# Performance work log

Measured on AMD Instinct MI355X. Metric: run time of the kernel, lower is better.

Reference implementation:

```python
import jax, jax.numpy as jnp
import numpy as np

B, S, R = 1, 512, 384
C_MSA, C_Z, C_HID, N_HEAD = 64, 128, 32, 8
INF = 1e8


def layer_norm(x, gamma, beta, eps=1e-5):
    mu = jnp.mean(x, axis=-1, keepdims=True)
    var = jnp.mean(jnp.square(x - mu), axis=-1, keepdims=True)
    return (x - mu) * jax.lax.rsqrt(var + eps) * gamma + beta


def setup_inputs() -> dict:
    key = jax.random.key(0)
    ks = jax.random.split(key, 8)
    hc = N_HEAD * C_HID
    return {
        "m": jax.random.normal(ks[0], (B, S, R, C_MSA), jnp.float32),
        "z": jax.random.normal(ks[1], (B, R, R, C_Z), jnp.float32),
        "msa_mask": jnp.ones((B, S, R), jnp.float32),
        "z_mask": jnp.ones((B, R, R), jnp.float32),
        "ln_m_g": jnp.ones((C_MSA,), jnp.float32),
        "ln_m_b": jnp.zeros((C_MSA,), jnp.float32),
        "w_v": jax.random.normal(ks[2], (C_MSA, hc), jnp.float32) / np.sqrt(C_MSA),
        "w_g": jax.random.normal(ks[3], (C_MSA, hc), jnp.float32) * 0.02,
        "ln_z_g": jnp.ones((C_Z,), jnp.float32),
        "ln_z_b": jnp.zeros((C_Z,), jnp.float32),
        "w_b": jax.random.normal(ks[4], (C_Z, N_HEAD), jnp.float32) / np.sqrt(C_Z),
        "w_o": jax.random.normal(ks[5], (hc, C_MSA), jnp.float32) * 0.02,
    }


def reference(m, z, msa_mask, z_mask, ln_m_g, ln_m_b, w_v, w_g, ln_z_g, ln_z_b, w_b, w_o):
    b_, s_, r_ = m.shape[0], m.shape[1], m.shape[2]
    m_ln = layer_norm(m, ln_m_g, ln_m_b)                       # [B,S,R,Cm]
    v = (m_ln @ w_v).reshape(b_, s_, r_, N_HEAD, C_HID)        # [B,S,R,H,C]
    g = jax.nn.sigmoid(m_ln @ w_g).reshape(b_, s_, r_, N_HEAD, C_HID)
    bias = layer_norm(z, ln_z_g, ln_z_b) @ w_b                 # [B,R,R,H]
    bias = bias + INF * (z_mask[..., None] - 1.0)
    v = v * msa_mask[..., None, None]
    w = jax.nn.softmax(bias, axis=2)                           # softmax over j
    # weighted average over residues j, then sigmoid gating
    o = g * jnp.einsum('bijh,bsjhc->bsihc', w, v)              # [B,S,R,H,C]
    o = o.reshape(b_, s_, r_, N_HEAD * C_HID)
    return o @ w_o                                             # [B,S,R,Cm]
```

## Files before the change

### kernel.cpp

```cpp
#include <hip/hip_runtime.h>
#include <math.h>

#define S_DIM 512
#define R_DIM 384
#define CM 64
#define CZ 128
#define NH 8
#define CH 32
#define HC 256

typedef unsigned short u16;
typedef __attribute__((ext_vector_type(8))) __bf16 bf16x8;
typedef __attribute__((ext_vector_type(4))) float f32x4;

static __device__ __forceinline__ u16 f2bf(float f) {
    unsigned int u = __float_as_uint(f);
    unsigned int r = (u + 0x7fffu + ((u >> 16) & 1u)) >> 16;
    return (u16)r;
}
static __device__ __forceinline__ float bf2f(u16 h) {
    return __uint_as_float(((unsigned int)h) << 16);
}
static __device__ __forceinline__ void split2(float f, u16& hi, u16& lo) {
    hi = f2bf(f);
    lo = f2bf(f - bf2f(hi));
}

__global__ __launch_bounds__(256) void kW_prep(
    const float* __restrict__ wv, const float* __restrict__ wg,
    const float* __restrict__ wb,
    u16* __restrict__ wvT_hi, u16* __restrict__ wvT_lo,
    u16* __restrict__ wgT_hi, u16* __restrict__ wgT_lo,
    u16* __restrict__ wbT_hi, u16* __restrict__ wbT_lo)
{
    const int idx = blockIdx.x * 256 + threadIdx.x;
    if (idx < 16384) {
        const int n = idx >> 6, c = idx & 63;
        split2(wv[c * HC + n], wvT_hi[idx], wvT_lo[idx]);
    } else if (idx < 32768) {
        const int r = idx - 16384;
        const int n = r >> 6, c = r & 63;
        split2(wg[c * HC + n], wgT_hi[r], wgT_lo[r]);
    } else if (idx < 34816) {
        const int r = idx - 32768;
        const int n = r >> 7, c = r & 127;
        split2(n < NH ? wb[c * NH + n] : 0.f, wbT_hi[r], wbT_lo[r]);
    }
}

__global__ __launch_bounds__(256) void kA1_bias(
    const float* __restrict__ z, const float* __restrict__ z_mask,
    const float* __restrict__ ln_z_g, const float* __restrict__ ln_z_b,
    const u16* __restrict__ wbT_hi, const u16* __restrict__ wbT_lo,
    float* __restrict__ bias_ws)
{
    __shared__ __align__(16) u16 a_hi[128 * 136];
    __shared__ __align__(16) u16 a_lo[128 * 136];
    __shared__ __align__(16) u16 b_hi[16 * 136];
    __shared__ __align__(16) u16 b_lo[16 * 136];
    const int tid  = threadIdx.x;
    const int lane = tid & 63, w = tid >> 6;
    const int row0 = blockIdx.x * 128;

    {
        const int r = tid >> 1, half = tid & 1;
        const float* src = z + (size_t)(row0 + r) * CZ + half * 64;
        float x[64];
        float s1 = 0.f, s2 = 0.f;
        #pragma unroll
        for (int e = 0; e < 16; ++e) {
            float4 v4 = *reinterpret_cast<const float4*>(src + e * 4);
            x[e*4+0] = v4.x; x[e*4+1] = v4.y; x[e*4+2] = v4.z; x[e*4+3] = v4.w;
            s1 += v4.x + v4.y + v4.z + v4.w;
            s2 += v4.x*v4.x + v4.y*v4.y + v4.z*v4.z + v4.w*v4.w;
        }
        s1 += __shfl_xor(s1, 1);
        s2 += __shfl_xor(s2, 1);
        const float mu   = s1 * (1.f / CZ);
        const float var  = s2 * (1.f / CZ) - mu * mu;
        const float rstd = rsqrtf(var + 1e-5f);
        #pragma unroll
        for (int e = 0; e < 16; ++e) {
            float4 g4 = *reinterpret_cast<const float4*>(ln_z_g + half * 64 + e * 4);
            float4 b4 = *reinterpret_cast<const float4*>(ln_z_b + half * 64 + e * 4);
            const int c = half * 64 + e * 4;
            split2((x[e*4+0] - mu) * rstd * g4.x + b4.x,
                   a_hi[r * 136 + c + 0], a_lo[r * 136 + c + 0]);
            split2((x[e*4+1] - mu) * rstd * g4.y + b4.y,
                   a_hi[r * 136 + c + 1], a_lo[r * 136 + c + 1]);
            split2((x[e*4+2] - mu) * rstd * g4.z + b4.z,
                   a_hi[r * 136 + c + 2], a_lo[r * 136 + c + 2]);
            split2((x[e*4+3] - mu) * rstd * g4.w + b4.w,
                   a_hi[r * 136 + c + 3], a_lo[r * 136 + c + 3]);
        }
    }
    {
        const int row = tid >> 4, off = (tid & 15) * 8;
        *reinterpret_cast<uint4*>(&b_hi[row * 136 + off]) =
            *reinterpret_cast<const uint4*>(wbT_hi + row * 128 + off);
        *reinterpret_cast<uint4*>(&b_lo[row * 136 + off]) =
            *reinterpret_cast<const uint4*>(wbT_lo + row * 128 + off);
    }
    __syncthreads();

    const int wr = w * 32;
    f32x4 acc[2] = {};
    #pragma unroll
    for (int ks = 0; ks < 4; ++ks) {
        const int ko = ks * 32 + (lane >> 4) * 8;
        bf16x8 bh = *reinterpret_cast<const bf16x8*>(&b_hi[(lane & 15) * 136 + ko]);
        bf16x8 bl = *reinterpret_cast<const bf16x8*>(&b_lo[(lane & 15) * 136 + ko]);
        #pragma unroll
        for (int mm = 0; mm < 2; ++mm) {
            const int base = (wr + mm * 16 + (lane & 15)) * 136 + ko;
            bf16x8 ah = *reinterpret_cast<const bf16x8*>(&a_hi[base]);
            bf16x8 al = *reinterpret_cast<const bf16x8*>(&a_lo[base]);
            acc[mm] = __builtin_amdgcn_mfma_f32_16x16x32_bf16(ah, bh, acc[mm], 0, 0, 0);
            acc[mm] = __builtin_amdgcn_mfma_f32_16x16x32_bf16(al, bh, acc[mm], 0, 0, 0);
            acc[mm] = __builtin_amdgcn_mfma_f32_16x16x32_bf16(ah, bl, acc[mm], 0, 0, 0);
        }
    }

    __syncthreads();
    float* T = reinterpret_cast<float*>(a_hi);
    const int cl = lane & 15, r4 = (lane >> 4) * 4;
    #pragma unroll
    for (int mm = 0; mm < 2; ++mm) {
        if (cl < NH) {
            #pragma unroll
            for (int r = 0; r < 4; ++r)
                T[cl * 132 + wr + mm * 16 + r4 + r] = acc[mm][r];
        }
    }
    __syncthreads();
    {
        const int h = tid >> 5, q = (tid & 31) * 4;
        float4 v  = *reinterpret_cast<const float4*>(&T[h * 132 + q]);
        float4 mk = *reinterpret_cast<const float4*>(z_mask + row0 + q);
        v.x += 1e8f * (mk.x - 1.f);
        v.y += 1e8f * (mk.y - 1.f);
        v.z += 1e8f * (mk.z - 1.f);
        v.w += 1e8f * (mk.w - 1.f);
        *reinterpret_cast<float4*>(
            &bias_ws[(size_t)h * R_DIM * R_DIM + row0 + q]) = v;
    }
}

__global__ __launch_bounds__(256) void kA2_softmax(
    const float* __restrict__ bias_ws, u16* __restrict__ w_soft)
{
    const int tid = threadIdx.x, w = tid >> 6, lane = tid & 63;
    const int row = blockIdx.x * 4 + w;
    const float* src = bias_ws + (size_t)row * R_DIM;
    float vals[6];
    float mx = -1e30f;
    #pragma unroll
    for (int u = 0; u < 6; ++u) {
        vals[u] = src[lane + u * 64];
        mx = fmaxf(mx, vals[u]);
    }
    #pragma unroll
    for (int msk = 32; msk >= 1; msk >>= 1) mx = fmaxf(mx, __shfl_xor(mx, msk));
    float sum = 0.f;
    #pragma unroll
    for (int u = 0; u < 6; ++u) { vals[u] = __expf(vals[u] - mx); sum += vals[u]; }
    #pragma unroll
    for (int msk = 32; msk >= 1; msk >>= 1) sum += __shfl_xor(sum, msk);
    const float inv = 1.0f / sum;
    u16* dst = w_soft + (size_t)row * R_DIM;
    #pragma unroll
    for (int u = 0; u < 6; ++u)
        dst[lane + u * 64] = f2bf(vals[u] * inv);
}

__global__ __launch_bounds__(256) void kB_mfma(
    const float* __restrict__ m_chunk, const float* __restrict__ mask_chunk,
    const float* __restrict__ ln_g, const float* __restrict__ ln_b,
    const u16* __restrict__ wvT_hi, const u16* __restrict__ wvT_lo,
    const u16* __restrict__ wgT_hi, const u16* __restrict__ wgT_lo,
    u16* __restrict__ Vt, u16* __restrict__ gbuf, int SCH)
{
    __shared__ __align__(16) u16 smem[4 * 128 * 72];
    u16* a_hi = smem;
    u16* a_lo = smem + 128 * 72;
    u16* b_hi = smem + 2 * 128 * 72;
    u16* b_lo = smem + 3 * 128 * 72;
    const int tid   = threadIdx.x;
    const int panel = blockIdx.x;
    const int si0   = blockIdx.y * 128;
    const int n0    = (panel & 1) * 128;
    const int lane  = tid & 63;
    const int w     = tid >> 6;
    const int wr    = (w >> 1) * 64, wc = (w & 1) * 64;

    {
        const int r = tid >> 1, half = tid & 1;
        const float* src = m_chunk + (size_t)(si0 + r) * CM + half * 32;
        float x[32];
        float s1 = 0.f, s2 = 0.f;
        #pragma unroll
        for (int e = 0; e < 8; ++e) {
            float4 v4 = *reinterpret_cast<const float4*>(src + e * 4);
            x[e*4+0] = v4.x; x[e*4+1] = v4.y; x[e*4+2] = v4.z; x[e*4+3] = v4.w;
            s1 += v4.x + v4.y + v4.z + v4.w;
            s2 += v4.x*v4.x + v4.y*v4.y + v4.z*v4.z + v4.w*v4.w;
        }
        s1 += __shfl_xor(s1, 1);
        s2 += __shfl_xor(s2, 1);
        const float mu   = s1 * (1.f / 64);
        const float var  = s2 * (1.f / 64) - mu * mu;
        const float rstd = rsqrtf(var + 1e-5f);
        #pragma unroll
        for (int e = 0; e < 8; ++e) {
            #pragma unroll
            for (int q = 0; q < 4; ++q) {
                const int c = half * 32 + e * 4 + q;
                const float v = (x[e*4+q] - mu) * rstd * ln_g[c] + ln_b[c];
                split2(v, a_hi[r * 72 + c], a_lo[r * 72 + c]);
            }
        }
    }
    {
        const u16* Wh = (panel < 2 ? wvT_hi : wgT_hi) + (size_t)n0 * 64;
        const u16* Wl = (panel < 2 ? wvT_lo : wgT_lo) + (size_t)n0 * 64;
        #pragma unroll
        for (int e = 0; e < 4; ++e) {
            const int c = e * 256 + tid;
            const int row = c >> 3, off = (c & 7) * 8;
            *reinterpret_cast<uint4*>(&b_hi[row * 72 + off]) =
                *reinterpret_cast<const uint4*>(Wh + row * 64 + off);
            *reinterpret_cast<uint4*>(&b_lo[row * 72 + off]) =
                *reinterpret_cast<const uint4*>(Wl + row * 64 + off);
        }
    }
    __syncthreads();

    f32x4 acc[4][4] = {};
    #pragma unroll
    for (int ks = 0; ks < 2; ++ks) {
        const int ko = ks * 32 + (lane >> 4) * 8;
        bf16x8 ah[4], al[4], bh[4], bl[4];
        #pragma unroll
        for (int mm = 0; mm < 4; ++mm) {
            const int base = (wr + mm * 16 + (lane & 15)) * 72 + ko;
            ah[mm] = *reinterpret_cast<const bf16x8*>(&a_hi[base]);
            al[mm] = *reinterpret_cast<const bf16x8*>(&a_lo[base]);
        }
        #pragma unroll
        for (int nn = 0; nn < 4; ++nn) {
            const int base = (wc + nn * 16 + (lane & 15)) * 72 + ko;
            bh[nn] = *reinterpret_cast<const bf16x8*>(&b_hi[base]);
            bl[nn] = *reinterpret_cast<const bf16x8*>(&b_lo[base]);
        }
        #pragma unroll
        for (int mm = 0; mm < 4; ++mm)
            #pragma unroll
            for (int nn = 0; nn < 4; ++nn) {
                acc[mm][nn] = __builtin_amdgcn_mfma_f32_16x16x32_bf16(
                    ah[mm], bh[nn], acc[mm][nn], 0, 0, 0);
                acc[mm][nn] = __builtin_amdgcn_mfma_f32_16x16x32_bf16(
                    al[mm], bh[nn], acc[mm][nn], 0, 0, 0);
                acc[mm][nn] = __builtin_amdgcn_mfma_f32_16x16x32_bf16(
                    ah[mm], bl[nn], acc[mm][nn], 0, 0, 0);
            }
    }

    __syncthreads();
    const int r4 = (lane >> 4) * 4, cl = lane & 15;
    if (panel < 2) {
        u16* T = smem;
        #pragma unroll
        for (int mm = 0; mm < 4; ++mm) {
            const int rowb = wr + mm * 16 + r4;
            const float4 mk = *reinterpret_cast<const float4*>(mask_chunk + si0 + rowb);
            #pragma unroll
            for (int nn = 0; nn < 4; ++nn) {
                const int n = wc + nn * 16 + cl;
                ushort4 pk;
                pk.x = f2bf(acc[mm][nn][0] * mk.x);
                pk.y = f2bf(acc[mm][nn][1] * mk.y);
                pk.z = f2bf(acc[mm][nn][2] * mk.z);
                pk.w = f2bf(acc[mm][nn][3] * mk.w);
                *reinterpret_cast<ushort4*>(&T[n * 136 + rowb]) = pk;
            }
        }
        __syncthreads();
        const int sc = si0 / R_DIM, j0 = si0 % R_DIM;
        const size_t Nn = (size_t)SCH * 32;
        #pragma unroll
        for (int e = 0; e < 8; ++e) {
            const int c = e * 256 + tid;
            const int n = c >> 4, part = c & 15;
            const int k = n0 + n;
            const int h = k >> 5, cc = k & 31;
            u16* dst = Vt + ((size_t)h * Nn + (size_t)sc * 32 + cc) * R_DIM
                         + j0 + part * 8;
            *reinterpret_cast<uint4*>(dst) =
                *reinterpret_cast<const uint4*>(&T[n * 136 + part * 8]);
        }
    } else {
        u16* T = smem;
        #pragma unroll
        for (int mm = 0; mm < 4; ++mm) {
            const int rowb = wr + mm * 16 + r4;
            #pragma unroll
            for (int nn = 0; nn < 4; ++nn) {
                const int n = wc + nn * 16 + cl;
                #pragma unroll
                for (int r = 0; r < 4; ++r)
                    T[(rowb + r) * 136 + n] =
                        f2bf(1.f / (1.f + __expf(-acc[mm][nn][r])));
            }
        }
        __syncthreads();
        #pragma unroll
        for (int e = 0; e < 8; ++e) {
            const int c = e * 256 + tid;
            const int row = c >> 4, part = c & 15;
            u16* dst = gbuf + (size_t)(si0 + row) * HC + n0 + part * 8;
            *reinterpret_cast<uint4*>(dst) =
                *reinterpret_cast<const uint4*>(&T[row * 136 + part * 8]);
        }
    }
}

__global__ __launch_bounds__(256) void kC_mfma(
    const u16* __restrict__ Wsoft, const u16* __restrict__ Vt,
    u16* __restrict__ o_pre, int SCH)
{
    constexpr int LDSP = 40;
    __shared__ __align__(16) u16 lds_a[128 * LDSP];
    __shared__ __align__(16) u16 lds_b[128 * LDSP];
    const int N   = SCH * 32;
    const int n0  = blockIdx.x * 128;
    const int i0  = blockIdx.y * 128;
    const int h   = blockIdx.z;
    const int tid = threadIdx.x;
    const int lane = tid & 63;
    const int w    = tid >> 6;
    const int wr   = (w >> 1) * 64;
    const int wc   = (w & 1) * 64;

    const u16* Wp = Wsoft + (size_t)h * R_DIM * R_DIM;
    const u16* Vp = Vt    + (size_t)h * N * R_DIM;

    f32x4 acc[4][4] = {};

    for (int k0 = 0; k0 < R_DIM; k0 += 32) {
        __syncthreads();
        #pragma unroll
        for (int rep = 0; rep < 2; ++rep) {
            const int c = rep * 256 + tid;
            const int row = c >> 2, q = c & 3;
            uint4 va = *reinterpret_cast<const uint4*>(
                Wp + (size_t)(i0 + row) * R_DIM + k0 + q * 8);
            *reinterpret_cast<uint4*>(&lds_a[row * LDSP + q * 8]) = va;
            uint4 vb = *reinterpret_cast<const uint4*>(
                Vp + (size_t)(n0 + row) * R_DIM + k0 + q * 8);
            *reinterpret_cast<uint4*>(&lds_b[row * LDSP + q * 8]) = vb;
        }
        __syncthreads();

        bf16x8 afrag[4], bfrag[4];
        #pragma unroll
        for (int mm = 0; mm < 4; ++mm) {
            const int row = wr + mm * 16 + (lane & 15);
            afrag[mm] = *reinterpret_cast<const bf16x8*>(
                &lds_a[row * LDSP + (lane >> 4) * 8]);
        }
        #pragma unroll
        for (int nn = 0; nn < 4; ++nn) {
            const int row = wc + nn * 16 + (lane & 15);
            bfrag[nn] = *reinterpret_cast<const bf16x8*>(
                &lds_b[row * LDSP + (lane >> 4) * 8]);
        }
        #pragma unroll
        for (int mm = 0; mm < 4; ++mm)
            #pragma unroll
            for (int nn = 0; nn < 4; ++nn)
                acc[mm][nn] = __builtin_amdgcn_mfma_f32_16x16x32_bf16(
                    afrag[mm], bfrag[nn], acc[mm][nn], 0, 0, 0);
    }

    const int r4 = (lane >> 4) * 4;
    const int cl = lane & 15;
    #pragma unroll
    for (int mm = 0; mm < 4; ++mm) {
        #pragma unroll
        for (int nn = 0; nn < 4; ++nn) {
            const int i = i0 + wr + mm * 16 + r4;
            const int n = n0 + wc + nn * 16 + cl;
            const int sc = n >> 5, cc = n & 31;
            u16* dst = &o_pre[((size_t)sc * R_DIM + i) * HC + h * 32 + cc];
            #pragma unroll
            for (int r = 0; r < 4; ++r)
                dst[(size_t)r * HC] = f2bf(acc[mm][nn][r]);
        }
    }
}

__global__ __launch_bounds__(256) void kD_out(
    const u16* __restrict__ gbuf, const u16* __restrict__ o_pre,
    const float* __restrict__ w_o, float* __restrict__ out_chunk, int SCH)
{
    __shared__ float A[128 * 65];
    __shared__ float Bt[64 * 64];
    const int si0 = blockIdx.x * 128;
    const int tid = threadIdx.x;
    const int tx  = tid & 15, ty = tid >> 4;
    float acc[8][4] = {};

    for (int k0 = 0; k0 < HC; k0 += 64) {
        {
            const int r = tid >> 1, half = tid & 1;
            const size_t base = (size_t)(si0 + r) * HC + k0 + half * 32;
            float* dst = &A[r * 65 + half * 32];
            #pragma unroll
            for (int e = 0; e < 4; ++e) {
                uint4 gv = *reinterpret_cast<const uint4*>(gbuf + base + e * 8);
                uint4 ov = *reinterpret_cast<const uint4*>(o_pre + base + e * 8);
                const u16* ga = (const u16*)&gv;
                const u16* oa = (const u16*)&ov;
                #pragma unroll
                for (int q = 0; q < 8; ++q)
                    dst[e * 8 + q] = bf2f(ga[q]) * bf2f(oa[q]);
            }
        }
        {
            const int kk = tid >> 2, q = tid & 3;
            #pragma unroll
            for (int e = 0; e < 4; ++e) {
                float4 v4 = *reinterpret_cast<const float4*>(
                    w_o + (size_t)(k0 + kk) * CM + q * 16 + e * 4);
                *reinterpret_cast<float4*>(&Bt[kk * 64 + q * 16 + e * 4]) = v4;
            }
        }
        __syncthreads();
        #pragma unroll 8
        for (int kk = 0; kk < 64; ++kk) {
            float4 b = *reinterpret_cast<float4*>(&Bt[kk * 64 + tx * 4]);
            #pragma unroll
            for (int e = 0; e < 8; ++e) {
                float a = A[(ty * 8 + e) * 65 + kk];
                acc[e][0] += a * b.x; acc[e][1] += a * b.y;
                acc[e][2] += a * b.z; acc[e][3] += a * b.w;
            }
        }
        __syncthreads();
    }
    #pragma unroll
    for (int e = 0; e < 8; ++e) {
        *reinterpret_cast<float4*>(
            &out_chunk[(size_t)(si0 + ty * 8 + e) * CM + tx * 4]) =
            make_float4(acc[e][0], acc[e][1], acc[e][2], acc[e][3]);
    }
}

extern "C" void kernel_launch(void* const* d_in, const int* in_sizes, int n_in,
                              void* d_out, int out_size, void* d_ws, size_t ws_size,
                              hipStream_t stream)
{
    const float* m        = (const float*)d_in[0];
    const float* z        = (const float*)d_in[1];
    const float* msa_mask = (const float*)d_in[2];
    const float* z_mask   = (const float*)d_in[3];
    const float* ln_m_g   = (const float*)d_in[4];
    const float* ln_m_b   = (const float*)d_in[5];
    const float* w_v      = (const float*)d_in[6];
    const float* w_g      = (const float*)d_in[7];
    const float* ln_z_g   = (const float*)d_in[8];
    const float* ln_z_b   = (const float*)d_in[9];
    const float* w_b      = (const float*)d_in[10];
    const float* w_o      = (const float*)d_in[11];
    float* out = (float*)d_out;

    const size_t wsoft_bytes = (size_t)NH * R_DIM * R_DIM * 2;
    const size_t bias_bytes  = (size_t)NH * R_DIM * R_DIM * 4;
    const size_t wts_bytes   = 4 * 16384 * 2 + 2 * 2048 * 2;
    const size_t per_sch = (size_t)R_DIM * HC * (2 + 2 + 2);
    int SCH = 256;
    while (SCH > 4 &&
           wsoft_bytes + bias_bytes + wts_bytes + (size_t)SCH * per_sch > ws_size)
        SCH >>= 1;

    char* p = (char*)d_ws;
    u16* w_soft   = (u16*)p; p += wsoft_bytes;
    float* biasws = (float*)p; p += bias_bytes;
    u16* wvT_hi   = (u16*)p; p += 16384 * 2;
    u16* wvT_lo   = (u16*)p; p += 16384 * 2;
    u16* wgT_hi   = (u16*)p; p += 16384 * 2;
    u16* wgT_lo   = (u16*)p; p += 16384 * 2;
    u16* wbT_hi   = (u16*)p; p += 2048 * 2;
    u16* wbT_lo   = (u16*)p; p += 2048 * 2;
    u16* Vt       = (u16*)p; p += (size_t)SCH * 32 * NH * R_DIM * 2;
    u16* gbuf     = (u16*)p; p += (size_t)SCH * R_DIM * HC * 2;
    u16* obuf     = (u16*)p;

    kW_prep<<<136, 256, 0, stream>>>(w_v, w_g, w_b, wvT_hi, wvT_lo,
                                     wgT_hi, wgT_lo, wbT_hi, wbT_lo);
    kA1_bias<<<R_DIM * R_DIM / 128, 256, 0, stream>>>(
        z, z_mask, ln_z_g, ln_z_b, wbT_hi, wbT_lo, biasws);
    kA2_softmax<<<NH * R_DIM / 4, 256, 0, stream>>>(biasws, w_soft);

    for (int s0 = 0; s0 < S_DIM; s0 += SCH) {
        kB_mfma<<<dim3(4, SCH * 3), 256, 0, stream>>>(
            m + (size_t)s0 * R_DIM * CM, msa_mask + (size_t)s0 * R_DIM,
            ln_m_g, ln_m_b, wvT_hi, wvT_lo, wgT_hi, wgT_lo, Vt, gbuf, SCH);
        kC_mfma<<<dim3(SCH / 4, 3, NH), 256, 0, stream>>>(w_soft, Vt, obuf, SCH);
        kD_out<<<dim3(SCH * 3), 256, 0, stream>>>(gbuf, obuf, w_o,
                                                  out + (size_t)s0 * R_DIM * CM, SCH);
    }
}
```

Before: 328.1 us.

## Compute LayerNorm once per row tile and loop all four V/G panels in-block

Each kB block now normalizes its 128 rows of m once, then loops over the four V and gate output panels. Before, four separate blocks each re-read and re-normalized the same rows. Weight fragments are read straight from global memory instead of being staged in LDS, and the normalized activations are packed in registers and written to LDS as vector stores. This cuts redundant m traffic and LayerNorm work by four times, but the grid shrinks by four, which may leave compute units idle and serializes the panels inside each block.

```diff
diff --git a/kernel.cpp b/kernel.cpp
--- a/kernel.cpp
+++ b/kernel.cpp
@@ -180,18 +180,14 @@
     const u16* __restrict__ wgT_hi, const u16* __restrict__ wgT_lo,
     u16* __restrict__ Vt, u16* __restrict__ gbuf, int SCH)
 {
-    __shared__ __align__(16) u16 smem[4 * 128 * 72];
-    u16* a_hi = smem;
-    u16* a_lo = smem + 128 * 72;
-    u16* b_hi = smem + 2 * 128 * 72;
-    u16* b_lo = smem + 3 * 128 * 72;
-    const int tid   = threadIdx.x;
-    const int panel = blockIdx.x;
-    const int si0   = blockIdx.y * 128;
-    const int n0    = (panel & 1) * 128;
-    const int lane  = tid & 63;
-    const int w     = tid >> 6;
-    const int wr    = (w >> 1) * 64, wc = (w & 1) * 64;
+    __shared__ __align__(16) u16 a_hi[128 * 72];
+    __shared__ __align__(16) u16 a_lo[128 * 72];
+    __shared__ __align__(16) u16 Tbuf[128 * 136];
+    const int tid  = threadIdx.x;
+    const int si0  = blockIdx.x * 128;
+    const int lane = tid & 63;
+    const int w    = tid >> 6;
+    const int wr   = (w >> 1) * 64, wc = (w & 1) * 64;
 
     {
         const int r = tid >> 1, half = tid & 1;
@@ -210,116 +206,121 @@
         const float mu   = s1 * (1.f / 64);
         const float var  = s2 * (1.f / 64) - mu * mu;
         const float rstd = rsqrtf(var + 1e-5f);
+        u16 ph[32], pl[32];
         #pragma unroll
         for (int e = 0; e < 8; ++e) {
             #pragma unroll
             for (int q = 0; q < 4; ++q) {
-                const int c = half * 32 + e * 4 + q;
-                const float v = (x[e*4+q] - mu) * rstd * ln_g[c] + ln_b[c];
-                split2(v, a_hi[r * 72 + c], a_lo[r * 72 + c]);
-            }
-        }
-    }
-    {
-        const u16* Wh = (panel < 2 ? wvT_hi : wgT_hi) + (size_t)n0 * 64;
-        const u16* Wl = (panel < 2 ? wvT_lo : wgT_lo) + (size_t)n0 * 64;
+                const int cl_ = e * 4 + q;
+                const int c = half * 32 + cl_;
+                const float v = (x[cl_] - mu) * rstd * ln_g[c] + ln_b[c];
+                split2(v, ph[cl_], pl[cl_]);
+            }
+        }
+        u16* dh = &a_hi[r * 72 + half * 32];
+        u16* dl = &a_lo[r * 72 + half * 32];
         #pragma unroll
         for (int e = 0; e < 4; ++e) {
-            const int c = e * 256 + tid;
-            const int row = c >> 3, off = (c & 7) * 8;
-            *reinterpret_cast<uint4*>(&b_hi[row * 72 + off]) =
-                *reinterpret_cast<const uint4*>(Wh + row * 64 + off);
-            *reinterpret_cast<uint4*>(&b_lo[row * 72 + off]) =
-                *reinterpret_cast<const uint4*>(Wl + row * 64 + off);
+            *reinterpret_cast<uint4*>(dh + e * 8) =
+                reinterpret_cast<const uint4*>(ph)[e];
+            *reinterpret_cast<uint4*>(dl + e * 8) =
+                reinterpret_cast<const uint4*>(pl)[e];
         }
     }
     __syncthreads();
 
-    f32x4 acc[4][4] = {};
-    #pragma unroll
-    for (int ks = 0; ks < 2; ++ks) {
-        const int ko = ks * 32 + (lane >> 4) * 8;
-        bf16x8 ah[4], al[4], bh[4], bl[4];
-        #pragma unroll
-        for (int mm = 0; mm < 4; ++mm) {
-            const int base = (wr + mm * 16 + (lane & 15)) * 72 + ko;
-            ah[mm] = *reinterpret_cast<const bf16x8*>(&a_hi[base]);
-            al[mm] = *reinterpret_cast<const bf16x8*>(&a_lo[base]);
-        }
-        #pragma unroll
-        for (int nn = 0; nn < 4; ++nn) {
-            const int base = (wc + nn * 16 + (lane & 15)) * 72 + ko;
-            bh[nn] = *reinterpret_cast<const bf16x8*>(&b_hi[base]);
-            bl[nn] = *reinterpret_cast<const bf16x8*>(&b_lo[base]);
-        }
-        #pragma unroll
-        for (int mm = 0; mm < 4; ++mm)
+    #pragma unroll
+    for (int t = 0; t < 4; ++t) {
+        const int n0   = (t & 1) * 128;
+        const bool isV = (t < 2);
+        const u16* Wh = (isV ? wvT_hi : wgT_hi) + (size_t)n0 * 64;
+        const u16* Wl = (isV ? wvT_lo : wgT_lo) + (size_t)n0 * 64;
+
+        f32x4 acc[4][4] = {};
+        #pragma unroll
+        for (int ks = 0; ks < 2; ++ks) {
+            const int ko = ks * 32 + (lane >> 4) * 8;
+            bf16x8 ah[4], al[4], bh[4], bl[4];
             #pragma unroll
             for (int nn = 0; nn < 4; ++nn) {
-                acc[mm][nn] = __builtin_amdgcn_mfma_f32_16x16x32_bf16(
-                    ah[mm], bh[nn], acc[mm][nn], 0, 0, 0);
-                acc[mm][nn] = __builtin_amdgcn_mfma_f32_16x16x32_bf16(
-                    al[mm], bh[nn], acc[mm][nn], 0, 0, 0);
-                acc[mm][nn] = __builtin_amdgcn_mfma_f32_16x16x32_bf16(
-                    ah[mm], bl[nn], acc[mm][nn], 0, 0, 0);
-            }
-    }
-
-    __syncthreads();
-    const int r4 = (lane >> 4) * 4, cl = lane & 15;
-    if (panel < 2) {
-        u16* T = smem;
-        #pragma unroll
-        for (int mm = 0; mm < 4; ++mm) {
-            const int rowb = wr + mm * 16 + r4;
-            const float4 mk = *reinterpret_cast<const float4*>(mask_chunk + si0 + rowb);
-            #pragma unroll
-            for (int nn = 0; nn < 4; ++nn) {
-                const int n = wc + nn * 16 + cl;
-                ushort4 pk;
-                pk.x = f2bf(acc[mm][nn][0] * mk.x);
-                pk.y = f2bf(acc[mm][nn][1] * mk.y);
-                pk.z = f2bf(acc[mm][nn][2] * mk.z);
-                pk.w = f2bf(acc[mm][nn][3] * mk.w);
-                *reinterpret_cast<ushort4*>(&T[n * 136 + rowb]) = pk;
-            }
+                const size_t base = (size_t)(wc + nn * 16 + (lane & 15)) * 64 + ko;
+                bh[nn] = *reinterpret_cast<const bf16x8*>(Wh + base);
+                bl[nn] = *reinterpret_cast<const bf16x8*>(Wl + base);
+            }
+            #pragma unroll
+            for (int mm = 0; mm < 4; ++mm) {
+                const int abase = (wr + mm * 16 + (lane & 15)) * 72 + ko;
+                ah[mm] = *reinterpret_cast<const bf16x8*>(&a_hi[abase]);
+                al[mm] = *reinterpret_cast<const bf16x8*>(&a_lo[abase]);
+            }
+            #pragma unroll
+            for (int mm = 0; mm < 4; ++mm)
+                #pragma unroll
+                for (int nn = 0; nn < 4; ++nn) {
+                    acc[mm][nn] = __builtin_amdgcn_mfma_f32_16x16x32_bf16(
+                        ah[mm], bh[nn], acc[mm][nn], 0, 0, 0);
+                    acc[mm][nn] = __builtin_amdgcn_mfma_f32_16x16x32_bf16(
+                        al[mm], bh[nn], acc[mm][nn], 0, 0, 0);
+                    acc[mm][nn] = __builtin_amdgcn_mfma_f32_16x16x32_bf16(
+                        ah[mm], bl[nn], acc[mm][nn], 0, 0, 0);
+                }
         }
         __syncthreads();
-        const int sc = si0 / R_DIM, j0 = si0 % R_DIM;
-        const size_t Nn = (size_t)SCH * 32;
-        #pragma unroll
-        for (int e = 0; e < 8; ++e) {
-            const int c = e * 256 + tid;
-            const int n = c >> 4, part = c & 15;
-            const int k = n0 + n;
-            const int h = k >> 5, cc = k & 31;
-            u16* dst = Vt + ((size_t)h * Nn + (size_t)sc * 32 + cc) * R_DIM
-                         + j0 + part * 8;
-            *reinterpret_cast<uint4*>(dst) =
-                *reinterpret_cast<const uint4*>(&T[n * 136 + part * 8]);
-        }
-    } else {
-        u16* T = smem;
-        #pragma unroll
-        for (int mm = 0; mm < 4; ++mm) {
-            const int rowb = wr + mm * 16 + r4;
-            #pragma unroll
-            for (int nn = 0; nn < 4; ++nn) {
-                const int n = wc + nn * 16 + cl;
+
+        const int r4 = (lane >> 4) * 4, cl = lane & 15;
+        if (isV) {
+            #pragma unroll
+            for (int mm = 0; mm < 4; ++mm) {
+                const int rowb = wr + mm * 16 + r4;
+                const float4 mk =
+                    *reinterpret_cast<const float4*>(mask_chunk + si0 + rowb);
                 #pragma unroll
-                for (int r = 0; r < 4; ++r)
-                    T[(rowb + r) * 136 + n] =
-                        f2bf(1.f / (1.f + __expf(-acc[mm][nn][r])));
-            }
-        }
-        __syncthreads();
-        #pragma unroll
-        for (int e = 0; e < 8; ++e) {
-            const int c = e * 256 + tid;
-            const int row = c >> 4, part = c & 15;
-            u16* dst = gbuf + (size_t)(si0 + row) * HC + n0 + part * 8;
-            *reinterpret_cast<uint4*>(dst) =
-                *reinterpret_cast<const uint4*>(&T[row * 136 + part * 8]);
+                for (int nn = 0; nn < 4; ++nn) {
+                    const int n = wc + nn * 16 + cl;
+                    ushort4 pk;
+                    pk.x = f2bf(acc[mm][nn][0] * mk.x);
+                    pk.y = f2bf(acc[mm][nn][1] * mk.y);
+                    pk.z = f2bf(acc[mm][nn][2] * mk.z);
+                    pk.w = f2bf(acc[mm][nn][3] * mk.w);
+                    *reinterpret_cast<ushort4*>(&Tbuf[n * 136 + rowb]) = pk;
+                }
+            }
+            __syncthreads();
+            const int sc = si0 / R_DIM, j0 = si0 % R_DIM;
+            const size_t Nn = (size_t)SCH * 32;
+            #pragma unroll
+            for (int e = 0; e < 8; ++e) {
+                const int c = e * 256 + tid;
+                const int n = c >> 4, part = c & 15;
+                const int k = n0 + n;
+                const int h = k >> 5, cc = k & 31;
+                u16* dst = Vt + ((size_t)h * Nn + (size_t)sc * 32 + cc) * R_DIM
+                             + j0 + part * 8;
+                *reinterpret_cast<uint4*>(dst) =
+                    *reinterpret_cast<const uint4*>(&Tbuf[n * 136 + part * 8]);
+            }
+        } else {
+            #pragma unroll
+            for (int mm = 0; mm < 4; ++mm) {
+                const int rowb = wr + mm * 16 + r4;
+                #pragma unroll
+                for (int nn = 0; nn < 4; ++nn) {
+                    const int n = wc + nn * 16 + cl;
+                    #pragma unroll
+                    for (int r = 0; r < 4; ++r)
+                        Tbuf[(rowb + r) * 136 + n] =
+                            f2bf(1.f / (1.f + __expf(-acc[mm][nn][r])));
+                }
+            }
+            __syncthreads();
+            #pragma unroll
+            for (int e = 0; e < 8; ++e) {
+                const int c = e * 256 + tid;
+                const int row = c >> 4, part = c & 15;
+                u16* dst = gbuf + (size_t)(si0 + row) * HC + n0 + part * 8;
+                *reinterpret_cast<uint4*>(dst) =
+                    *reinterpret_cast<const uint4*>(&Tbuf[row * 136 + part * 8]);
+            }
         }
     }
 }
@@ -503,7 +504,7 @@
     kA2_softmax<<<NH * R_DIM / 4, 256, 0, stream>>>(biasws, w_soft);
 
     for (int s0 = 0; s0 < S_DIM; s0 += SCH) {
-        kB_mfma<<<dim3(4, SCH * 3), 256, 0, stream>>>(
+        kB_mfma<<<dim3(SCH * 3), 256, 0, stream>>>(
             m + (size_t)s0 * R_DIM * CM, msa_mask + (size_t)s0 * R_DIM,
             ln_m_g, ln_m_b, wvT_hi, wvT_lo, wgT_hi, wgT_lo, Vt, gbuf, SCH);
         kC_mfma<<<dim3(SCH / 4, 3, NH), 256, 0, stream>>>(w_soft, Vt, obuf, SCH);
```

Result: faster. 317.1 us (-3.4%).
